# Optimization experiments

Measured on AMD Instinct MI355X. Metric: run time of the kernel, lower is better.

## Reference

```python
import jax, jax.numpy as jnp
import numpy as np

BETA = 0.25

def setup_inputs() -> dict:
    key = jax.random.key(0)
    k1, k2 = jax.random.split(key)
    z = jax.random.normal(k1, (16, 256, 32, 32), dtype=jnp.float32)
    # embedding initialized uniform(-1/ne, 1/ne) in the module; scale is immaterial for correctness
    ne = 8192
    codebook = jax.random.uniform(k2, (ne, 256), dtype=jnp.float32, minval=-1.0 / ne, maxval=1.0 / ne)
    return {"z": z, "codebook": codebook}


def reference(z, codebook):
    # z: [B, C, H, W] channel-first -> channel-last [B, H, W, C]
    z_cl = jnp.transpose(z, (0, 2, 3, 1))
    # distance (up to a constant ||z||^2 term, as in the original):
    # d = ||e||^2 - 2 <z, e>, shape [B, H, W, NE]
    d = jnp.sum(codebook ** 2, axis=1) - 2.0 * jnp.einsum('bhwd,nd->bhwn', z_cl, codebook)
    index = jnp.argmin(d, axis=-1)                      # [B, H, W]
    z_q = codebook[index]                               # [B, H, W, C] gather
    # commitment + codebook losses with straight-through
    loss = jnp.mean((jax.lax.stop_gradient(z_q) - z_cl) ** 2) \
         + BETA * jnp.mean((z_q - jax.lax.stop_gradient(z_cl)) ** 2)
    z_q_st = z_cl + jax.lax.stop_gradient(z_q - z_cl)   # straight-through estimator
    z_q_cf = jnp.transpose(z_q_st, (0, 3, 1, 2))        # back to channel-first [B, C, H, W]
    return z_q_cf, index, loss
```

## Files before the change

### kernel.cpp

```cpp
#include <hip/hip_runtime.h>
#include <float.h>

#define NPIX 16384
#define NE   8192
#define KD   256
#define HW   1024
#define BCHW 262144
#define NT   8
#define DELTA 2.5e-4f
#define KMASK 0xFFFFE000u

typedef __attribute__((ext_vector_type(8))) short short8;
typedef __attribute__((ext_vector_type(4))) short short4v;
typedef __attribute__((ext_vector_type(4))) float f32x4;
typedef __attribute__((ext_vector_type(4))) unsigned int u32x4;
typedef unsigned long long u64;
typedef unsigned int u32;

__device__ __forceinline__ u32 fkey(float f) {
    u32 u = __float_as_uint(f);
    return u ^ ((u >> 31) ? 0xFFFFFFFFu : 0x80000000u);
}
__device__ __forceinline__ short bf16rne(float f) {
    u32 u = __float_as_uint(f);
    u += 0x7FFFu + ((u >> 16) & 1u);
    return (short)(u >> 16);
}
__device__ __forceinline__ float kval(u32 pk) {
    return __uint_as_float(pk & KMASK);
}

#define GLDS(gp, lp) __builtin_amdgcn_global_load_lds( \
    (const __attribute__((address_space(1))) void*)(gp), \
    (__attribute__((address_space(3))) void*)(lp), 16, 0, 0)

__global__ __launch_bounds__(256) void vq_prep2(
    const float* __restrict__ cb, const float* __restrict__ z,
    short* __restrict__ eh, float* __restrict__ e2, short* __restrict__ zh)
{
    __shared__ float ts[64][65];
    const int tid = threadIdx.x;

    if (blockIdx.x < 2048) {
        const int row  = ((int)blockIdx.x * 256 + tid) >> 6;
        const int lane = tid & 63;
        const f32x4 v = *(const f32x4*)(cb + (size_t)row * KD + lane * 4);
        short4v h;
        h[0] = bf16rne(v[0]); h[1] = bf16rne(v[1]);
        h[2] = bf16rne(v[2]); h[3] = bf16rne(v[3]);
        *(short4v*)(eh + (size_t)row * KD + lane * 4) = h;
        float s = v[0]*v[0] + v[1]*v[1] + v[2]*v[2] + v[3]*v[3];
        #pragma unroll
        for (int m = 1; m < 64; m <<= 1) s += __shfl_xor(s, m);
        if (lane == 0) e2[row] = s;
    } else {
        const int bid = (int)blockIdx.x - 2048;
        const int hw0 = (bid & 15) * 64;
        const int k0  = ((bid >> 4) & 3) * 64;
        const int b   = bid >> 6;
        const int pl  = tid & 63, kk = tid >> 6;
        #pragma unroll
        for (int i = 0; i < 16; ++i) {
            const int k = kk + 4 * i;
            ts[k][pl] = z[b * BCHW + (k0 + k) * HW + hw0 + pl];
        }
        __syncthreads();
        const int tx = tid & 15, ty = tid >> 4;
        #pragma unroll
        for (int j = 0; j < 4; ++j) {
            const int p = ty + 16 * j;
            short4v v;
            #pragma unroll
            for (int q = 0; q < 4; ++q) v[q] = bf16rne(ts[tx * 4 + q][p]);
            *(short4v*)(zh + (size_t)(b * HW + hw0 + p) * KD + k0 + tx * 4) = v;
        }
    }
}

__global__ __launch_bounds__(512, 2) void vq_gemm(
    const short* __restrict__ zh, const short* __restrict__ eh,
    u32* __restrict__ best4)
{
    __shared__ short Bs[4][4096];

    const int tid  = threadIdx.x;
    const int lane = tid & 63;
    const int w    = tid >> 6;
    const int wm   = w >> 1, wn = w & 1;
    const int lr   = lane & 15;
    const int p0   = blockIdx.x * 128;
    const int nb0  = blockIdx.y * (NT * 128);

    const int sr = lane >> 2;
    const int ss = (lane & 3) ^ ((sr >> 1) & 3);
    const int q   = lane >> 4;
    const int rsw = (lr >> 1) & 3;

    u32 b1[2][4], b2[2][4];
    #pragma unroll
    for (int m = 0; m < 2; ++m)
        #pragma unroll
        for (int r = 0; r < 4; ++r) { b1[m][r] = 0xFFFFFFFFu; b2[m][r] = 0xFFFFFFFFu; }

    short8 afr[2][8];
    #pragma unroll
    for (int m = 0; m < 2; ++m) {
        const size_t rowb = (size_t)(p0 + wm * 32 + m * 16 + lr) * KD;
        #pragma unroll
        for (int ks = 0; ks < 8; ++ks)
            afr[m][ks] = *(const short8*)(zh + rowb + ks * 32 + q * 8);
    }
    asm volatile("s_waitcnt vmcnt(0)" ::: "memory");

    #define STAGEB(nt_, t_, buf_) do {                                         \
        const int k0_ = (t_) * 32;                                             \
        const int n0_ = nb0 + (nt_) * 128;                                     \
        GLDS(eh + (size_t)(n0_ + w * 16 + sr) * KD + k0_ + ss * 8,             \
             &Bs[buf_][w * 512]);                                              \
    } while (0)

    f32x4 acc[2][4];

    STAGEB(0, 0, 0);
    STAGEB(0, 1, 1);

    #pragma unroll 1
    for (int nt = 0; nt < NT; ++nt) {
        const bool lastnt = (nt == NT - 1);
        #pragma unroll
        for (int t = 0; t < 8; ++t) {
            if (lastnt && t == 7) asm volatile("s_waitcnt vmcnt(0)" ::: "memory");
            else                  asm volatile("s_waitcnt vmcnt(1)" ::: "memory");
            __builtin_amdgcn_sched_barrier(0);
            __builtin_amdgcn_s_barrier();

            if (t < 6)        { STAGEB(nt, t + 2, (t + 2) & 3); }
            else if (!lastnt) { STAGEB(nt + 1, t - 6, (t - 6) & 3); }

            if (t == 0) {
                #pragma unroll
                for (int m = 0; m < 2; ++m)
                    #pragma unroll
                    for (int nf = 0; nf < 4; ++nf)
                        acc[m][nf] = (f32x4){0.f, 0.f, 0.f, 0.f};
            }

            short8 bfv[4];
            #pragma unroll
            for (int nf = 0; nf < 4; ++nf) {
                const int row = wn * 64 + nf * 16 + lr;
                bfv[nf] = *(const short8*)&Bs[t & 3][row * 32 + ((q ^ rsw) * 8)];
            }
            #pragma unroll
            for (int m = 0; m < 2; ++m)
                #pragma unroll
                for (int nf = 0; nf < 4; ++nf)
                    acc[m][nf] = __builtin_amdgcn_mfma_f32_16x16x32_bf16(
                        afr[m][t], bfv[nf], acc[m][nf], 0, 0, 0);

            if (t == 7) {
                const u32 nbase = (u32)(nb0 + nt * 128 + wn * 64 + lr);
                #pragma unroll
                for (int m = 0; m < 2; ++m) {
                    #pragma unroll
                    for (int r = 0; r < 4; ++r) {
                        u32 pk0 = (__float_as_uint(0.0625f - acc[m][0][r]) & KMASK) | (nbase);
                        u32 pk1 = (__float_as_uint(0.0625f - acc[m][1][r]) & KMASK) | (nbase + 16u);
                        u32 pk2 = (__float_as_uint(0.0625f - acc[m][2][r]) & KMASK) | (nbase + 32u);
                        u32 pk3 = (__float_as_uint(0.0625f - acc[m][3][r]) & KMASK) | (nbase + 48u);
                        const u32 lo01 = min(pk0, pk1), hi01 = max(pk0, pk1);
                        const u32 lo23 = min(pk2, pk3), hi23 = max(pk2, pk3);
                        const u32 m1 = min(lo01, lo23);
                        const u32 m2 = min(max(lo01, lo23), min(hi01, hi23));
                        const u32 nb1 = min(b1[m][r], m1);
                        const u32 nb2 = min(max(b1[m][r], m1), min(b2[m][r], m2));
                        b1[m][r] = nb1; b2[m][r] = nb2;
                    }
                }
            }
        }
    }
    #undef STAGEB

    const int g = lane >> 4;
    const int hs = blockIdx.y * 2 + wn;
    #pragma unroll
    for (int m = 0; m < 2; ++m) {
        #pragma unroll
        for (int r = 0; r < 4; ++r) {
            u32 a = b1[m][r], b = b2[m][r];
            u32 o[4];
            #pragma unroll
            for (int j = 0; j < 4; ++j) {
                u32 mm = a;
                #pragma unroll
                for (int msk = 1; msk < 16; msk <<= 1)
                    mm = min(mm, (u32)__shfl_xor((int)mm, msk));
                o[j] = mm;
                if (a == mm) { a = b; b = 0xFFFFFFFFu; }
            }
            if (lr == 0) {
                const int prow = p0 + wm * 32 + m * 16 + g * 4 + r;
                u32x4 ov; ov[0] = o[0]; ov[1] = o[1]; ov[2] = o[2]; ov[3] = o[3];
                *(u32x4*)&best4[((size_t)prow * 16 + hs) * 4] = ov;
            }
        }
    }
}

__global__ __launch_bounds__(256) void vq_out_kernel(
    const float* __restrict__ z, const float* __restrict__ cb,
    const float* __restrict__ e2, const u32* __restrict__ best4,
    float* __restrict__ out, float* __restrict__ idxf,
    float* __restrict__ loss)
{
    __shared__ float zb[32][260];
    __shared__ float zq[32][257];
    __shared__ u64  sfinal[32];
    __shared__ int  nidx[32];
    __shared__ u32  work[2048];
    __shared__ u32  scans[512];
    __shared__ int  nwork, nscan;

    const int tid = threadIdx.x;
    const int p0  = blockIdx.x * 32;
    const int bb  = p0 >> 10, hw0 = p0 & 1023;

    if (tid == 0) { nwork = 0; nscan = 0; }
    if (tid < 32) sfinal[tid] = ~0ULL;
    __syncthreads();

    {
        const int pix = tid >> 3;
        const int hp  = (tid & 7) * 2;
        const u32* src = &best4[((size_t)(p0 + pix) * 16 + hp) * 4];
        const u32x4 kv0 = *(const u32x4*)(src);
        const u32x4 kv1 = *(const u32x4*)(src + 4);
        u32 lmin = min(min(kv0[0], kv0[1]), min(kv0[2], kv0[3]));
        lmin = min(lmin, min(min(kv1[0], kv1[1]), min(kv1[2], kv1[3])));
        u32 mn = lmin;
        #pragma unroll
        for (int m = 1; m < 8; m <<= 1) mn = min(mn, (u32)__shfl_xor((int)mn, m));
        const float thr = kval(mn) + DELTA;
        int c8 = 0;
        #pragma unroll
        for (int j = 0; j < 4; ++j) c8 += (kval(kv0[j]) <= thr) ? 1 : 0;
        #pragma unroll
        for (int j = 0; j < 4; ++j) c8 += (kval(kv1[j]) <= thr) ? 1 : 0;
        int cnt = c8;
        #pragma unroll
        for (int m = 1; m < 8; m <<= 1) cnt += __shfl_xor(cnt, m);
        const int s0 = (kval(kv0[3]) <= thr) ? 1 : 0;
        const int s1 = (kval(kv1[3]) <= thr) ? 1 : 0;
        int anysusp = s0 + s1;
        #pragma unroll
        for (int m = 1; m < 8; m <<= 1) anysusp += __shfl_xor(anysusp, m);

        if (cnt == 1 && anysusp == 0) {
            if (lmin == mn) sfinal[pix] = (u64)(mn & 8191u);
        } else {
            if (c8 > 0) {
                const int base = atomicAdd(&nwork, c8);
                int k = 0;
                #pragma unroll
                for (int j = 0; j < 4; ++j)
                    if (kval(kv0[j]) <= thr)
                        work[base + (k++)] = ((u32)pix << 13) | (kv0[j] & 8191u);
                #pragma unroll
                for (int j = 0; j < 4; ++j)
                    if (kval(kv1[j]) <= thr)
                        work[base + (k++)] = ((u32)pix << 13) | (kv1[j] & 8191u);
            }
            if (s0) scans[atomicAdd(&nscan, 1)] = ((u32)pix << 4) | (u32)hp;
            if (s1) scans[atomicAdd(&nscan, 1)] = ((u32)pix << 4) | (u32)(hp + 1);
        }
    }
    __syncthreads();

    #pragma unroll
    for (int i = 0; i < 32; ++i) {
        const int idx = i * 256 + tid;
        const int c = idx >> 5, px = idx & 31;
        zb[px][c] = z[(size_t)bb * BCHW + (size_t)c * HW + hw0 + px];
    }
    __syncthreads();

    const int nw = nwork, ns = nscan;

    for (int i = tid; i < nw; i += 256) {
        const u32 e = work[i];
        const int px = (int)(e >> 13), n = (int)(e & 8191u);
        const float* er = cb + (size_t)n * KD;
        float acc = 0.f;
        #pragma unroll 4
        for (int k = 0; k < KD; k += 4) {
            const f32x4 zv = *(const f32x4*)&zb[px][k];
            const f32x4 ev = *(const f32x4*)(er + k);
            acc += zv[0]*ev[0] + zv[1]*ev[1] + zv[2]*ev[2] + zv[3]*ev[3];
        }
        const float s = 0.5f * e2[n] - acc;
        atomicMin(&sfinal[px], ((u64)fkey(s) << 32) | (u32)n);
    }

    for (int si = 0; si < ns; ++si) {
        const u32 e = scans[si];
        const int px = (int)(e >> 4), hx = (int)(e & 15u);
        u64 bku = ~0ULL;
        #pragma unroll
        for (int h = 0; h < 2; ++h) {
            const int ci = tid + h * 256;
            const int n = (hx >> 1) * 1024 + (ci >> 6) * 128
                        + (hx & 1) * 64 + (ci & 63);
            const float* er = cb + (size_t)n * KD;
            float acc = 0.f;
            #pragma unroll 4
            for (int k = 0; k < KD; k += 4) {
                const f32x4 zv = *(const f32x4*)&zb[px][k];
                const f32x4 ev = *(const f32x4*)(er + k);
                acc += zv[0]*ev[0] + zv[1]*ev[1] + zv[2]*ev[2] + zv[3]*ev[3];
            }
            const float s = 0.5f * e2[n] - acc;
            const u64 pk = ((u64)fkey(s) << 32) | (u32)n;
            bku = min(bku, pk);
        }
        #pragma unroll
        for (int m = 1; m < 64; m <<= 1) {
            const u64 o = (u64)__shfl_xor((long long)bku, m);
            bku = min(bku, o);
        }
        if ((tid & 63) == 0) atomicMin(&sfinal[px], bku);
    }
    __syncthreads();

    if (tid < 32) {
        const int n = (int)((u32)sfinal[tid] & 8191u);
        nidx[tid] = n;
        idxf[p0 + tid] = (float)n;
    }
    __syncthreads();

    {
        const int r = tid >> 3, i = tid & 7;
        const float* src = cb + (size_t)nidx[r] * KD;
        #pragma unroll
        for (int j = 0; j < 8; ++j) {
            const int col = i * 4 + j * 32;
            const f32x4 v = *(const f32x4*)(src + col);
            zq[r][col + 0] = v[0]; zq[r][col + 1] = v[1];
            zq[r][col + 2] = v[2]; zq[r][col + 3] = v[3];
        }
    }
    __syncthreads();

    const int p4 = (tid & 7) * 4;
    const int cg = tid >> 3;
    float ls = 0.f;
    #pragma unroll
    for (int ii = 0; ii < 8; ++ii) {
        const int c = cg + 32 * ii;
        const size_t e = (size_t)bb * BCHW + (size_t)c * HW + hw0 + p4;
        f32x4 v;
        v[0] = zq[p4 + 0][c]; v[1] = zq[p4 + 1][c];
        v[2] = zq[p4 + 2][c]; v[3] = zq[p4 + 3][c];
        *(f32x4*)(out + e) = v;
        const float d0 = v[0] - zb[p4 + 0][c], d1 = v[1] - zb[p4 + 1][c];
        const float d2 = v[2] - zb[p4 + 2][c], d3 = v[3] - zb[p4 + 3][c];
        ls += d0 * d0 + d1 * d1 + d2 * d2 + d3 * d3;
    }
    #pragma unroll
    for (int m = 1; m < 64; m <<= 1) ls += __shfl_xor(ls, m);
    if ((tid & 63) == 0) atomicAdd(loss, ls * (1.25f / 4194304.f));
}

extern "C" void kernel_launch(void* const* d_in, const int* in_sizes, int n_in,
                              void* d_out, int out_size, void* d_ws, size_t ws_size,
                              hipStream_t stream) {
    const float* z  = (const float*)d_in[0];
    const float* cb = (const float*)d_in[1];
    float* out  = (float*)d_out;
    float* idxf = out + 4194304;
    float* loss = out + 4210688;
    char* ob = (char*)d_out;
    short* zh    = (short*)ob;
    short* eh    = (short*)(ob + 8388608);
    u32*   best4 = (u32*)(ob + 12582912);

    float* e2 = (float*)d_ws;

    hipMemsetAsync(loss, 0, 4, stream);

    vq_prep2<<<3072, 256, 0, stream>>>(cb, z, eh, e2, zh);
    vq_gemm<<<dim3(NPIX / 128, NE / (NT * 128)), 512, 0, stream>>>(zh, eh, best4);
    vq_out_kernel<<<NPIX / 32, 256, 0, stream>>>(z, cb, e2, best4, out, idxf, loss);
}
```

Before: 178.2 us.

## Software-pipeline LDS B-fragment reads one k-step ahead of MFMAs

The inner loop now reads the B fragments for step t from shared memory into a double-buffered register set, while the MFMAs consume the fragments loaded in the previous step. Each tile's final MFMA and its top-2 merge move to the start of the next tile, with an epilogue after the loop for the last tile. This is meant to hide LDS read latency behind matrix work. The MFMA groups are also wrapped in s_setprio raises to favour issue of this wave. The cost is more vector registers for the second B buffer and more complex control flow.

```diff
diff --git a/kernel.cpp b/kernel.cpp
--- a/kernel.cpp
+++ b/kernel.cpp
@@ -119,7 +119,57 @@
              &Bs[buf_][w * 512]);                                              \
     } while (0)
 
+    #define READB(buf_, reg_) do {                                             \
+        _Pragma("unroll")                                                      \
+        for (int nf_ = 0; nf_ < 4; ++nf_) {                                    \
+            const int row_ = wn * 64 + nf_ * 16 + lr;                          \
+            bfv[reg_][nf_] =                                                   \
+                *(const short8*)&Bs[buf_][row_ * 32 + ((q ^ rsw) * 8)];        \
+        }                                                                      \
+    } while (0)
+
+    #define DOMFMA(tc_, reg_) do {                                             \
+        __builtin_amdgcn_s_setprio(1);                                         \
+        _Pragma("unroll")                                                      \
+        for (int m_ = 0; m_ < 2; ++m_)                                         \
+            _Pragma("unroll")                                                  \
+            for (int nf_ = 0; nf_ < 4; ++nf_)                                  \
+                acc[m_][nf_] = __builtin_amdgcn_mfma_f32_16x16x32_bf16(        \
+                    afr[m_][tc_], bfv[reg_][nf_], acc[m_][nf_], 0, 0, 0);      \
+        __builtin_amdgcn_s_setprio(0);                                         \
+    } while (0)
+
+    #define MERGE(ntc_) do {                                                   \
+        const u32 nbase = (u32)(nb0 + (ntc_) * 128 + wn * 64 + lr);            \
+        _Pragma("unroll")                                                      \
+        for (int m_ = 0; m_ < 2; ++m_) {                                       \
+            _Pragma("unroll")                                                  \
+            for (int r_ = 0; r_ < 4; ++r_) {                                   \
+                u32 pk0 = (__float_as_uint(0.0625f - acc[m_][0][r_]) & KMASK) | (nbase);        \
+                u32 pk1 = (__float_as_uint(0.0625f - acc[m_][1][r_]) & KMASK) | (nbase + 16u);  \
+                u32 pk2 = (__float_as_uint(0.0625f - acc[m_][2][r_]) & KMASK) | (nbase + 32u);  \
+                u32 pk3 = (__float_as_uint(0.0625f - acc[m_][3][r_]) & KMASK) | (nbase + 48u);  \
+                const u32 lo01 = min(pk0, pk1), hi01 = max(pk0, pk1);          \
+                const u32 lo23 = min(pk2, pk3), hi23 = max(pk2, pk3);          \
+                const u32 m1 = min(lo01, lo23);                                \
+                const u32 m2 = min(max(lo01, lo23), min(hi01, hi23));          \
+                const u32 nb1 = min(b1[m_][r_], m1);                           \
+                const u32 nb2 = min(max(b1[m_][r_], m1), min(b2[m_][r_], m2)); \
+                b1[m_][r_] = nb1; b2[m_][r_] = nb2;                            \
+            }                                                                  \
+        }                                                                      \
+    } while (0)
+
+    #define ZEROACC() do {                                                     \
+        _Pragma("unroll")                                                      \
+        for (int m_ = 0; m_ < 2; ++m_)                                         \
+            _Pragma("unroll")                                                  \
+            for (int nf_ = 0; nf_ < 4; ++nf_)                                  \
+                acc[m_][nf_] = (f32x4){0.f, 0.f, 0.f, 0.f};                    \
+    } while (0)
+
     f32x4 acc[2][4];
+    short8 bfv[2][4];
 
     STAGEB(0, 0, 0);
     STAGEB(0, 1, 1);
@@ -137,50 +187,27 @@
             if (t < 6)        { STAGEB(nt, t + 2, (t + 2) & 3); }
             else if (!lastnt) { STAGEB(nt + 1, t - 6, (t - 6) & 3); }
 
+            READB(t & 3, t & 1);
+
             if (t == 0) {
-                #pragma unroll
-                for (int m = 0; m < 2; ++m)
-                    #pragma unroll
-                    for (int nf = 0; nf < 4; ++nf)
-                        acc[m][nf] = (f32x4){0.f, 0.f, 0.f, 0.f};
+                if (nt > 0) {
+                    DOMFMA(7, 1);
+                    MERGE(nt - 1);
+                }
+            } else {
+                if (t == 1) ZEROACC();
+                DOMFMA(t - 1, (t - 1) & 1);
             }
-
-            short8 bfv[4];
-            #pragma unroll
-            for (int nf = 0; nf < 4; ++nf) {
-                const int row = wn * 64 + nf * 16 + lr;
-                bfv[nf] = *(const short8*)&Bs[t & 3][row * 32 + ((q ^ rsw) * 8)];
-            }
-            #pragma unroll
-            for (int m = 0; m < 2; ++m)
-                #pragma unroll
-                for (int nf = 0; nf < 4; ++nf)
-                    acc[m][nf] = __builtin_amdgcn_mfma_f32_16x16x32_bf16(
-                        afr[m][t], bfv[nf], acc[m][nf], 0, 0, 0);
-
-            if (t == 7) {
-                const u32 nbase = (u32)(nb0 + nt * 128 + wn * 64 + lr);
-                #pragma unroll
-                for (int m = 0; m < 2; ++m) {
-                    #pragma unroll
-                    for (int r = 0; r < 4; ++r) {
-                        u32 pk0 = (__float_as_uint(0.0625f - acc[m][0][r]) & KMASK) | (nbase);
-                        u32 pk1 = (__float_as_uint(0.0625f - acc[m][1][r]) & KMASK) | (nbase + 16u);
-                        u32 pk2 = (__float_as_uint(0.0625f - acc[m][2][r]) & KMASK) | (nbase + 32u);
-                        u32 pk3 = (__float_as_uint(0.0625f - acc[m][3][r]) & KMASK) | (nbase + 48u);
-                        const u32 lo01 = min(pk0, pk1), hi01 = max(pk0, pk1);
-                        const u32 lo23 = min(pk2, pk3), hi23 = max(pk2, pk3);
-                        const u32 m1 = min(lo01, lo23);
-                        const u32 m2 = min(max(lo01, lo23), min(hi01, hi23));
-                        const u32 nb1 = min(b1[m][r], m1);
-                        const u32 nb2 = min(max(b1[m][r], m1), min(b2[m][r], m2));
-                        b1[m][r] = nb1; b2[m][r] = nb2;
-                    }
-                }
-            }
         }
     }
     #undef STAGEB
+
+    DOMFMA(7, 1);
+    MERGE(7);
+    #undef READB
+    #undef DOMFMA
+    #undef MERGE
+    #undef ZEROACC
 
     const int g = lane >> 4;
     const int hs = blockIdx.y * 2 + wn;
```

Measured after the change: 173.9 us. 1.02x faster.
